# Kernel tuning notes

Hardware: AMD Instinct MI355X
Metric: run time of the kernel (lower is better)

The kernel has to match this reference:

```python
import jax, jax.numpy as jnp
import numpy as np

S = 512       # number of rnn_output rows (source positions)
T = 512       # number of target rows (queries)
DU = 512      # dim_u
DT = 512      # dim_target
D = DU + DT   # concat dim


def setup_inputs() -> dict:
    key = jax.random.key(0)
    k1, k2, k3, k4, k5, k6 = jax.random.split(key, 6)
    return {
        "rnn_outputs": jax.random.normal(k1, (S, DU), dtype=jnp.float32),
        "target": jax.random.normal(k2, (T, DT), dtype=jnp.float32),
        # nn.Linear(D, D): weight [D, D], bias [D]
        "W_lin": jax.random.normal(k3, (D, D), dtype=jnp.float32) * 0.02,
        "b_lin": jax.random.normal(k4, (D,), dtype=jnp.float32) * 0.02,
        # nn.Linear(D, 1): weight [1, D] stored flat, bias scalar
        "w_score": jax.random.normal(k5, (D,), dtype=jnp.float32) * 0.02,
        "b_score": jax.random.normal(k6, (), dtype=jnp.float32) * 0.02,
    }


def reference(rnn_outputs, target, W_lin, b_lin, w_score, b_score):
    du = rnn_outputs.shape[1]
    # linear(concat([rnn, tgt])) == rnn @ W[:, :du].T + tgt @ W[:, du:].T + b
    # (split the weight instead of materializing the [T, S, D] concat)
    A = rnn_outputs @ W_lin[:, :du].T            # [S, D]
    B = target @ W_lin[:, du:].T + b_lin         # [T, D]
    h = jnp.tanh(B[:, None, :] + A[None, :, :])  # [T, S, D]
    scores = h @ w_score + b_score               # [T, S]
    weights = jax.nn.softmax(scores, axis=1)     # softmax over source dim S
    # stack of per-row weighted sums == weights @ rnn_outputs
    return weights @ rnn_outputs                 # [T, dim_u]
```

## Files before the change

kernel.cpp:

```cpp
#include <hip/hip_runtime.h>


#define C2F 2.8853900817779268f

typedef __attribute__((ext_vector_type(8))) short short8;
typedef __attribute__((ext_vector_type(4))) float f32x4;

__device__ __forceinline__ unsigned short bf16_rne(float f) {
    unsigned u = __builtin_bit_cast(unsigned, f);
    unsigned r = (u + 0x7FFFu + ((u >> 16) & 1u)) >> 16;
    return (unsigned short)r;
}
__device__ __forceinline__ float bf16_f(unsigned short h) {
    unsigned u = ((unsigned)h) << 16;
    return __builtin_bit_cast(float, u);
}

__global__ __launch_bounds__(256, 4) void k1_mfma(
    const float* __restrict__ rnn, const float* __restrict__ tgt,
    const float* __restrict__ W, const float* __restrict__ bl,
    float* __restrict__ Abuf, float* __restrict__ Bbuf, int ksplit)
{
    __shared__ unsigned short Xh[64][40], Xl[64][40], Wh[64][40], Wl[64][40];
    const int j0 = blockIdx.x * 64;
    const int i0 = blockIdx.y * 64;
    const int kz = blockIdx.z;
    const int klen = 512 / ksplit;
    const int kbase = kz * klen;
    const bool isB = (i0 >= 512);
    const float* __restrict__ X = isB ? tgt : rnn;
    const int irow0 = isB ? (i0 - 512) : i0;
    const int koff = isB ? 512 : 0;
    const int tid = threadIdx.x;
    const int lane = tid & 63;
    const int wv = tid >> 6;
    const int isub = (wv & 1) * 32;
    const int jsub = (wv >> 1) * 32;
    const int srow = tid >> 2;
    const int skq  = tid & 3;
    const float* __restrict__ xp = X + (size_t)(irow0 + srow) * 512 + kbase + skq * 8;
    const float* __restrict__ wp = W + (size_t)(j0 + srow) * 1024 + koff + kbase + skq * 8;
    const int frow = lane & 15;
    const int fk   = (lane >> 4) * 8;
    f32x4 acc00 = {0.f,0.f,0.f,0.f}, acc01 = {0.f,0.f,0.f,0.f};
    f32x4 acc10 = {0.f,0.f,0.f,0.f}, acc11 = {0.f,0.f,0.f,0.f};
    float4 xv0 = *(const float4*)(xp);
    float4 xv1 = *(const float4*)(xp + 4);
    float4 wv0 = *(const float4*)(wp);
    float4 wv1 = *(const float4*)(wp + 4);
    for (int k0 = 0; k0 < klen; k0 += 32) {
        __syncthreads();
        {
            short8 xh8, xl8, wh8, wl8;
            const float xf[8] = {xv0.x, xv0.y, xv0.z, xv0.w, xv1.x, xv1.y, xv1.z, xv1.w};
            const float wf[8] = {wv0.x, wv0.y, wv0.z, wv0.w, wv1.x, wv1.y, wv1.z, wv1.w};
            #pragma unroll
            for (int e = 0; e < 8; ++e) {
                const unsigned short xh = bf16_rne(xf[e]);
                const unsigned short wh = bf16_rne(wf[e]);
                xh8[e] = (short)xh;
                wh8[e] = (short)wh;
                xl8[e] = (short)bf16_rne(xf[e] - bf16_f(xh));
                wl8[e] = (short)bf16_rne(wf[e] - bf16_f(wh));
            }
            *(short8*)&Xh[srow][skq * 8] = xh8;
            *(short8*)&Xl[srow][skq * 8] = xl8;
            *(short8*)&Wh[srow][skq * 8] = wh8;
            *(short8*)&Wl[srow][skq * 8] = wl8;
        }
        __syncthreads();
        if (k0 + 32 < klen) {
            xv0 = *(const float4*)(xp + k0 + 32);
            xv1 = *(const float4*)(xp + k0 + 36);
            wv0 = *(const float4*)(wp + k0 + 32);
            wv1 = *(const float4*)(wp + k0 + 36);
        }
        const short8 ah0 = *(const short8*)&Xh[isub + frow][fk];
        const short8 ah1 = *(const short8*)&Xh[isub + 16 + frow][fk];
        const short8 bh0 = *(const short8*)&Wh[jsub + frow][fk];
        const short8 bh1 = *(const short8*)&Wh[jsub + 16 + frow][fk];
        acc00 = __builtin_amdgcn_mfma_f32_16x16x32_bf16(ah0, bh0, acc00, 0, 0, 0);
        acc01 = __builtin_amdgcn_mfma_f32_16x16x32_bf16(ah0, bh1, acc01, 0, 0, 0);
        acc10 = __builtin_amdgcn_mfma_f32_16x16x32_bf16(ah1, bh0, acc10, 0, 0, 0);
        acc11 = __builtin_amdgcn_mfma_f32_16x16x32_bf16(ah1, bh1, acc11, 0, 0, 0);
        const short8 al0 = *(const short8*)&Xl[isub + frow][fk];
        const short8 al1 = *(const short8*)&Xl[isub + 16 + frow][fk];
        acc00 = __builtin_amdgcn_mfma_f32_16x16x32_bf16(al0, bh0, acc00, 0, 0, 0);
        acc01 = __builtin_amdgcn_mfma_f32_16x16x32_bf16(al0, bh1, acc01, 0, 0, 0);
        acc10 = __builtin_amdgcn_mfma_f32_16x16x32_bf16(al1, bh0, acc10, 0, 0, 0);
        acc11 = __builtin_amdgcn_mfma_f32_16x16x32_bf16(al1, bh1, acc11, 0, 0, 0);
        const short8 bl0 = *(const short8*)&Wl[jsub + frow][fk];
        const short8 bl1 = *(const short8*)&Wl[jsub + 16 + frow][fk];
        acc00 = __builtin_amdgcn_mfma_f32_16x16x32_bf16(ah0, bl0, acc00, 0, 0, 0);
        acc01 = __builtin_amdgcn_mfma_f32_16x16x32_bf16(ah0, bl1, acc01, 0, 0, 0);
        acc10 = __builtin_amdgcn_mfma_f32_16x16x32_bf16(ah1, bl0, acc10, 0, 0, 0);
        acc11 = __builtin_amdgcn_mfma_f32_16x16x32_bf16(ah1, bl1, acc11, 0, 0, 0);
    }
    const int orow = (lane >> 4) * 4;
    const int ocol = lane & 15;
    float* __restrict__ dst = (isB ? Bbuf : Abuf) + (size_t)kz * 524288;
    const bool addb = isB && (kz == ksplit - 1);
#define K1ST(ACC, MT, NT) do {                                            \
    const int jl = jsub + (NT)*16 + ocol;                                 \
    const float bb = addb ? bl[j0 + jl] : 0.f;                            \
    const int il = isub + (MT)*16 + orow;                                 \
    float* p = dst + (size_t)(irow0 + il) * 1024 + j0 + jl;               \
    p[0]    = (ACC[0] + bb) * C2F;                                        \
    p[1024] = (ACC[1] + bb) * C2F;                                        \
    p[2048] = (ACC[2] + bb) * C2F;                                        \
    p[3072] = (ACC[3] + bb) * C2F;                                        \
} while (0)
    K1ST(acc00, 0, 0); K1ST(acc01, 0, 1); K1ST(acc10, 1, 0); K1ST(acc11, 1, 1);
#undef K1ST
}

__global__ __launch_bounds__(256, 4) void k1_gemm_ab(
    const float* __restrict__ rnn, const float* __restrict__ tgt,
    const float* __restrict__ W, const float* __restrict__ bl,
    float* __restrict__ Abuf, float* __restrict__ Bbuf, int ksplit, int doexp)
{
    __shared__ float xt[32][68];
    __shared__ float wt[32][68];
    const int j0 = blockIdx.x * 64;
    const int i0 = blockIdx.y * 64;
    const int kz = blockIdx.z;
    const int klen = 512 / ksplit;
    const int kbase = kz * klen;
    const bool isB = (i0 >= 512);
    const float* __restrict__ in = isB ? tgt : rnn;
    const int irow0 = isB ? (i0 - 512) : i0;
    const int koff = isB ? 512 : 0;
    const int tid = threadIdx.x;
    const int lrow = tid >> 2;
    const int kq   = tid & 3;
    const int ti   = tid >> 4;
    const int tj   = tid & 15;
    const float* __restrict__ inp = in + (size_t)(irow0 + lrow) * 512 + kbase + kq * 8;
    const float* __restrict__ wp  = W  + (size_t)(j0 + lrow) * 1024 + koff + kbase + kq * 8;
    float acc[4][4] = {};
    float4 x0 = *(const float4*)(inp);
    float4 x1 = *(const float4*)(inp + 4);
    float4 w0 = *(const float4*)(wp);
    float4 w1 = *(const float4*)(wp + 4);
    for (int k0 = 0; k0 < klen; k0 += 32) {
        __syncthreads();
        xt[kq*8+0][lrow] = x0.x; xt[kq*8+1][lrow] = x0.y; xt[kq*8+2][lrow] = x0.z; xt[kq*8+3][lrow] = x0.w;
        xt[kq*8+4][lrow] = x1.x; xt[kq*8+5][lrow] = x1.y; xt[kq*8+6][lrow] = x1.z; xt[kq*8+7][lrow] = x1.w;
        wt[kq*8+0][lrow] = w0.x; wt[kq*8+1][lrow] = w0.y; wt[kq*8+2][lrow] = w0.z; wt[kq*8+3][lrow] = w0.w;
        wt[kq*8+4][lrow] = w1.x; wt[kq*8+5][lrow] = w1.y; wt[kq*8+6][lrow] = w1.z; wt[kq*8+7][lrow] = w1.w;
        __syncthreads();
        if (k0 + 32 < klen) {
            x0 = *(const float4*)(inp + k0 + 32);
            x1 = *(const float4*)(inp + k0 + 36);
            w0 = *(const float4*)(wp + k0 + 32);
            w1 = *(const float4*)(wp + k0 + 36);
        }
        #pragma unroll
        for (int k = 0; k < 32; ++k) {
            const float4 av = *(const float4*)&xt[k][ti * 4];
            const float4 bv = *(const float4*)&wt[k][tj * 4];
            const float ar[4] = {av.x, av.y, av.z, av.w};
            const float br[4] = {bv.x, bv.y, bv.z, bv.w};
            #pragma unroll
            for (int r = 0; r < 4; ++r)
                #pragma unroll
                for (int c = 0; c < 4; ++c)
                    acc[r][c] = __builtin_fmaf(ar[r], br[c], acc[r][c]);
        }
    }
    float4 bq = make_float4(0.f, 0.f, 0.f, 0.f);
    if (isB && kz == ksplit - 1) bq = *(const float4*)(bl + j0 + tj * 4);
    float* __restrict__ dst = (isB ? Bbuf : Abuf) + (size_t)kz * 524288;
    #pragma unroll
    for (int r = 0; r < 4; ++r) {
        float4 o;
        o.x = (acc[r][0] + bq.x) * C2F;
        o.y = (acc[r][1] + bq.y) * C2F;
        o.z = (acc[r][2] + bq.z) * C2F;
        o.w = (acc[r][3] + bq.w) * C2F;
        if (doexp) {
            o.x = __builtin_amdgcn_exp2f(o.x);
            o.y = __builtin_amdgcn_exp2f(o.y);
            o.z = __builtin_amdgcn_exp2f(o.z);
            o.w = __builtin_amdgcn_exp2f(o.w);
        }
        *(float4*)(dst + (size_t)(irow0 + ti * 4 + r) * 1024 + j0 + tj * 4) = o;
    }
}

__global__ __launch_bounds__(256, 4) void k1b_sum(float* __restrict__ ws4)
{
    const int i = (blockIdx.x * 256 + threadIdx.x) * 4;
    const float4 a0 = *(const float4*)(ws4 + i);
    const float4 a1 = *(const float4*)(ws4 + 524288 + i);
    const float4 b0 = *(const float4*)(ws4 + 2 * 524288 + i);
    const float4 b1 = *(const float4*)(ws4 + 3 * 524288 + i);
    float4 a, b;
    a.x = __builtin_amdgcn_exp2f(a0.x + a1.x);
    a.y = __builtin_amdgcn_exp2f(a0.y + a1.y);
    a.z = __builtin_amdgcn_exp2f(a0.z + a1.z);
    a.w = __builtin_amdgcn_exp2f(a0.w + a1.w);
    b.x = __builtin_amdgcn_exp2f(b0.x + b1.x);
    b.y = __builtin_amdgcn_exp2f(b0.y + b1.y);
    b.z = __builtin_amdgcn_exp2f(b0.z + b1.z);
    b.w = __builtin_amdgcn_exp2f(b0.w + b1.w);
    *(float4*)(ws4 + i) = a;
    *(float4*)(ws4 + 2 * 524288 + i) = b;
}

#define K2CELL(ACC, CC, RR) do {                                         \
    const float e0_ = __builtin_fmaf(A0.CC, B0.RR, 1.f);                 \
    const float e1_ = __builtin_fmaf(A1.CC, B1.RR, 1.f);                 \
    const float e2_ = __builtin_fmaf(A2.CC, B2.RR, 1.f);                 \
    const float e3_ = __builtin_fmaf(A3.CC, B3.RR, 1.f);                 \
    const float l01_ = e0_ * e1_;                                        \
    const float l23_ = e2_ * e3_;                                        \
    const float n01_ = __builtin_fmaf(wa.x, e1_, wa.y * e0_);            \
    const float n23_ = __builtin_fmaf(wa.z, e3_, wa.w * e2_);            \
    const float N_ = __builtin_fmaf(n01_, l23_, n23_ * l01_);            \
    ACC = __builtin_fmaf(N_, __builtin_amdgcn_rcpf(l01_ * l23_), ACC);   \
} while (0)

__global__ __launch_bounds__(256, 4) void k2_scores(
    const float* __restrict__ EA, const float* __restrict__ EB,
    const float* __restrict__ wsc, float* __restrict__ P, int dchunk)
{
    __shared__ float at[32][68];
    __shared__ float bt[32][68];
    __shared__ float wl[128];
    const int s0 = blockIdx.x * 64;
    const int t0 = blockIdx.y * 64;
    const int dz = blockIdx.z * dchunk;
    const int tid = threadIdx.x;
    if (tid < dchunk) wl[tid] = wsc[dz + tid];
    const int srow = tid & 63;
    const int kq   = tid >> 6;
    const int ti   = tid >> 4;
    const int tj   = tid & 15;
    const float* __restrict__ Arow = EA + (size_t)(s0 + srow) * 1024 + dz + kq * 8;
    const float* __restrict__ Brow = EB + (size_t)(t0 + srow) * 1024 + dz + kq * 8;
    float4 acc0 = make_float4(0.f,0.f,0.f,0.f);
    float4 acc1 = make_float4(0.f,0.f,0.f,0.f);
    float4 acc2 = make_float4(0.f,0.f,0.f,0.f);
    float4 acc3 = make_float4(0.f,0.f,0.f,0.f);
    float4 pa0 = *(const float4*)(Arow);
    float4 pa1 = *(const float4*)(Arow + 4);
    float4 pb0 = *(const float4*)(Brow);
    float4 pb1 = *(const float4*)(Brow + 4);
    for (int d0 = 0; d0 < dchunk; d0 += 32) {
        __syncthreads();
        at[kq*8+0][srow] = pa0.x; at[kq*8+1][srow] = pa0.y; at[kq*8+2][srow] = pa0.z; at[kq*8+3][srow] = pa0.w;
        at[kq*8+4][srow] = pa1.x; at[kq*8+5][srow] = pa1.y; at[kq*8+6][srow] = pa1.z; at[kq*8+7][srow] = pa1.w;
        bt[kq*8+0][srow] = pb0.x; bt[kq*8+1][srow] = pb0.y; bt[kq*8+2][srow] = pb0.z; bt[kq*8+3][srow] = pb0.w;
        bt[kq*8+4][srow] = pb1.x; bt[kq*8+5][srow] = pb1.y; bt[kq*8+6][srow] = pb1.z; bt[kq*8+7][srow] = pb1.w;
        __syncthreads();
        if (d0 + 32 < dchunk) {
            pa0 = *(const float4*)(Arow + d0 + 32);
            pa1 = *(const float4*)(Arow + d0 + 36);
            pb0 = *(const float4*)(Brow + d0 + 32);
            pb1 = *(const float4*)(Brow + d0 + 36);
        }
        for (int dd = 0; dd < 32; dd += 4) {
            const float4 wa = *(const float4*)&wl[d0 + dd];
            const float4 A0 = *(const float4*)&at[dd + 0][tj * 4];
            const float4 A1 = *(const float4*)&at[dd + 1][tj * 4];
            const float4 A2 = *(const float4*)&at[dd + 2][tj * 4];
            const float4 A3 = *(const float4*)&at[dd + 3][tj * 4];
            const float4 B0 = *(const float4*)&bt[dd + 0][ti * 4];
            const float4 B1 = *(const float4*)&bt[dd + 1][ti * 4];
            const float4 B2 = *(const float4*)&bt[dd + 2][ti * 4];
            const float4 B3 = *(const float4*)&bt[dd + 3][ti * 4];
            K2CELL(acc0.x, x, x); K2CELL(acc0.y, y, x); K2CELL(acc0.z, z, x); K2CELL(acc0.w, w, x);
            K2CELL(acc1.x, x, y); K2CELL(acc1.y, y, y); K2CELL(acc1.z, z, y); K2CELL(acc1.w, w, y);
            K2CELL(acc2.x, x, z); K2CELL(acc2.y, y, z); K2CELL(acc2.z, z, z); K2CELL(acc2.w, w, z);
            K2CELL(acc3.x, x, w); K2CELL(acc3.y, y, w); K2CELL(acc3.z, z, w); K2CELL(acc3.w, w, w);
        }
    }
    float* __restrict__ Pz = P + (size_t)blockIdx.z * 512 * 512;
    *(float4*)(Pz + (size_t)(t0 + ti * 4 + 0) * 512 + s0 + tj * 4) = acc0;
    *(float4*)(Pz + (size_t)(t0 + ti * 4 + 1) * 512 + s0 + tj * 4) = acc1;
    *(float4*)(Pz + (size_t)(t0 + ti * 4 + 2) * 512 + s0 + tj * 4) = acc2;
    *(float4*)(Pz + (size_t)(t0 + ti * 4 + 3) * 512 + s0 + tj * 4) = acc3;
}

__global__ __launch_bounds__(256, 4) void k3_softmax(
    const float* __restrict__ P, float* __restrict__ wgt, int nz)
{
    __shared__ float wm[4];
    __shared__ float wsum[4];
    const int t = blockIdx.x;
    const int tid = threadIdx.x;
    const size_t base = (size_t)t * 512 + tid * 2;
    float sx = 0.f, sy = 0.f;
    for (int z = 0; z < nz; ++z) {
        const float2 p = *(const float2*)(P + base + (size_t)z * 262144);
        sx += p.x; sy += p.y;
    }
    const float x0 = -2.f * sx;
    const float x1 = -2.f * sy;
    float m = fmaxf(x0, x1);
    #pragma unroll
    for (int off = 32; off; off >>= 1) m = fmaxf(m, __shfl_xor(m, off));
    if ((tid & 63) == 0) wm[tid >> 6] = m;
    __syncthreads();
    m = fmaxf(fmaxf(wm[0], wm[1]), fmaxf(wm[2], wm[3]));
    const float L2E = 1.4426950408889634f;
    const float e0 = __builtin_amdgcn_exp2f((x0 - m) * L2E);
    const float e1 = __builtin_amdgcn_exp2f((x1 - m) * L2E);
    float s = e0 + e1;
    #pragma unroll
    for (int off = 32; off; off >>= 1) s += __shfl_xor(s, off);
    if ((tid & 63) == 0) wsum[tid >> 6] = s;
    __syncthreads();
    s = wsum[0] + wsum[1] + wsum[2] + wsum[3];
    const float inv = 1.0f / s;
    float2 o; o.x = e0 * inv; o.y = e1 * inv;
    *(float2*)(wgt + (size_t)t * 512 + tid * 2) = o;
}

__global__ __launch_bounds__(256, 4) void k4_out(
    const float* __restrict__ wgt, const float* __restrict__ rnn,
    float* __restrict__ P4)
{
    __shared__ float wtt[32][68];
    __shared__ float rn[32][68];
    const int d0g = blockIdx.x * 64;
    const int t0g = blockIdx.y * 64;
    const int z   = blockIdx.z;
    const int tid = threadIdx.x;
    const int trow = tid & 63;
    const int kq   = tid >> 6;
    const int srw  = tid & 31;
    const int cq   = tid >> 5;
    const int ti = tid >> 4, tj = tid & 15;
    float acc[4][4] = {};
    for (int sc = z * 64; sc < z * 64 + 64; sc += 32) {
        const float4 w0 = *(const float4*)(wgt + (size_t)(t0g + trow) * 512 + sc + kq * 8);
        const float4 w1 = *(const float4*)(wgt + (size_t)(t0g + trow) * 512 + sc + kq * 8 + 4);
        const float4 r0 = *(const float4*)(rnn + (size_t)(sc + srw) * 512 + d0g + cq * 8);
        const float4 r1 = *(const float4*)(rnn + (size_t)(sc + srw) * 512 + d0g + cq * 8 + 4);
        __syncthreads();
        wtt[kq*8+0][trow] = w0.x; wtt[kq*8+1][trow] = w0.y; wtt[kq*8+2][trow] = w0.z; wtt[kq*8+3][trow] = w0.w;
        wtt[kq*8+4][trow] = w1.x; wtt[kq*8+5][trow] = w1.y; wtt[kq*8+6][trow] = w1.z; wtt[kq*8+7][trow] = w1.w;
        *(float4*)&rn[srw][cq * 8]     = r0;
        *(float4*)&rn[srw][cq * 8 + 4] = r1;
        __syncthreads();
        #pragma unroll
        for (int s = 0; s < 32; ++s) {
            const float4 av = *(const float4*)&wtt[s][ti * 4];
            const float4 bv = *(const float4*)&rn[s][tj * 4];
            const float ar[4] = {av.x, av.y, av.z, av.w};
            const float bc[4] = {bv.x, bv.y, bv.z, bv.w};
            #pragma unroll
            for (int r = 0; r < 4; ++r)
                #pragma unroll
                for (int c = 0; c < 4; ++c)
                    acc[r][c] = __builtin_fmaf(ar[r], bc[c], acc[r][c]);
        }
    }
    float* __restrict__ Pz = P4 + (size_t)z * 262144;
    #pragma unroll
    for (int r = 0; r < 4; ++r) {
        float4 o;
        o.x = acc[r][0]; o.y = acc[r][1]; o.z = acc[r][2]; o.w = acc[r][3];
        *(float4*)(Pz + (size_t)(t0g + ti * 4 + r) * 512 + d0g + tj * 4) = o;
    }
}

__global__ __launch_bounds__(256, 4) void k5_reduce(
    const float* __restrict__ P4, float* __restrict__ out)
{
    const int i = (blockIdx.x * 256 + threadIdx.x) * 4;
    float4 a = *(const float4*)(P4 + i);
    #pragma unroll
    for (int z = 1; z < 8; ++z) {
        const float4 b = *(const float4*)(P4 + (size_t)z * 262144 + i);
        a.x += b.x; a.y += b.y; a.z += b.z; a.w += b.w;
    }
    *(float4*)(out + i) = a;
}

extern "C" void kernel_launch(void* const* d_in, const int* in_sizes, int n_in,
                              void* d_out, int out_size, void* d_ws, size_t ws_size,
                              hipStream_t stream) {
    const float* rnn = (const float*)d_in[0];
    const float* tgt = (const float*)d_in[1];
    const float* W   = (const float*)d_in[2];
    const float* bl  = (const float*)d_in[3];
    const float* wsc = (const float*)d_in[4];
    float* out = (float*)d_out;

    const int nz = 8;
    const int dchunk = 1024 / nz;
    float* ws = (float*)d_ws;

    const bool split = (ws_size >= 17825792u);

    if (split) {
        float* A   = ws;
        float* B   = ws + 2 * 524288;
        float* P   = ws + 4 * 524288;
        float* wgt = P + (size_t)nz * 262144;
        float* P4  = P;
        k1_mfma   <<<dim3(16, 16, 2), 256, 0, stream>>>(rnn, tgt, W, bl, A, B, 2);
        k1b_sum   <<<512,             256, 0, stream>>>(ws);
        k2_scores <<<dim3(8, 8, nz),  256, 0, stream>>>(A, B, wsc, P, dchunk);
        k3_softmax<<<512,             256, 0, stream>>>(P, wgt, nz);
        k4_out    <<<dim3(8, 8, 8),   256, 0, stream>>>(wgt, rnn, P4);
        k5_reduce <<<256,             256, 0, stream>>>(P4, out);
    } else {
        float* A   = ws;
        float* B   = ws + 524288;
        float* P   = ws + 2 * 524288;
        float* wgt = P + (size_t)nz * 262144;
        float* P4  = P;
        k1_gemm_ab<<<dim3(16, 16, 1), 256, 0, stream>>>(rnn, tgt, W, bl, A, B, 1, 1);
        k2_scores <<<dim3(8, 8, nz),  256, 0, stream>>>(A, B, wsc, P, dchunk);
        k3_softmax<<<512,             256, 0, stream>>>(P, wgt, nz);
        k4_out    <<<dim3(8, 8, 8),   256, 0, stream>>>(wgt, rnn, P4);
        k5_reduce <<<256,             256, 0, stream>>>(P4, out);
    }
}
```

Before: 59.96 us.

## Fuse split-K sum and exp into score kernel; use bf16x3 MFMA for output GEMM

Removes the separate k1b_sum kernel. The score kernel now loads both split-K partials of A and B, adds them, and applies exp2 while staging into shared memory. This saves one launch and a full read-write pass over the workspace, but the exp is now recomputed in every score block that reads the same data. The weights@rnn kernel is also rewritten to use bf16 MFMA with hi/lo splitting (three products) in place of scalar FMA, trading conversion overhead for matrix-core throughput.

```diff
diff --git a/kernel.cpp b/kernel.cpp
--- a/kernel.cpp
+++ b/kernel.cpp
@@ -188,26 +188,6 @@
     }
 }
 
-__global__ __launch_bounds__(256, 4) void k1b_sum(float* __restrict__ ws4)
-{
-    const int i = (blockIdx.x * 256 + threadIdx.x) * 4;
-    const float4 a0 = *(const float4*)(ws4 + i);
-    const float4 a1 = *(const float4*)(ws4 + 524288 + i);
-    const float4 b0 = *(const float4*)(ws4 + 2 * 524288 + i);
-    const float4 b1 = *(const float4*)(ws4 + 3 * 524288 + i);
-    float4 a, b;
-    a.x = __builtin_amdgcn_exp2f(a0.x + a1.x);
-    a.y = __builtin_amdgcn_exp2f(a0.y + a1.y);
-    a.z = __builtin_amdgcn_exp2f(a0.z + a1.z);
-    a.w = __builtin_amdgcn_exp2f(a0.w + a1.w);
-    b.x = __builtin_amdgcn_exp2f(b0.x + b1.x);
-    b.y = __builtin_amdgcn_exp2f(b0.y + b1.y);
-    b.z = __builtin_amdgcn_exp2f(b0.z + b1.z);
-    b.w = __builtin_amdgcn_exp2f(b0.w + b1.w);
-    *(float4*)(ws4 + i) = a;
-    *(float4*)(ws4 + 2 * 524288 + i) = b;
-}
-
 #define K2CELL(ACC, CC, RR) do {                                         \
     const float e0_ = __builtin_fmaf(A0.CC, B0.RR, 1.f);                 \
     const float e1_ = __builtin_fmaf(A1.CC, B1.RR, 1.f);                 \
@@ -221,9 +201,12 @@
     ACC = __builtin_fmaf(N_, __builtin_amdgcn_rcpf(l01_ * l23_), ACC);   \
 } while (0)
 
+#define K2EXP(P0, P1) __builtin_amdgcn_exp2f(__builtin_fmaf(sumf, (P1), (P0)))
+
 __global__ __launch_bounds__(256, 4) void k2_scores(
-    const float* __restrict__ EA, const float* __restrict__ EB,
-    const float* __restrict__ wsc, float* __restrict__ P, int dchunk)
+    const float* __restrict__ A0p, const float* __restrict__ A1p,
+    const float* __restrict__ B0p, const float* __restrict__ B1p,
+    const float* __restrict__ wsc, float* __restrict__ P, int dchunk, float sumf)
 {
     __shared__ float at[32][68];
     __shared__ float bt[32][68];
@@ -237,28 +220,50 @@
     const int kq   = tid >> 6;
     const int ti   = tid >> 4;
     const int tj   = tid & 15;
-    const float* __restrict__ Arow = EA + (size_t)(s0 + srow) * 1024 + dz + kq * 8;
-    const float* __restrict__ Brow = EB + (size_t)(t0 + srow) * 1024 + dz + kq * 8;
+    const float* __restrict__ Ar0 = A0p + (size_t)(s0 + srow) * 1024 + dz + kq * 8;
+    const float* __restrict__ Ar1 = A1p + (size_t)(s0 + srow) * 1024 + dz + kq * 8;
+    const float* __restrict__ Br0 = B0p + (size_t)(t0 + srow) * 1024 + dz + kq * 8;
+    const float* __restrict__ Br1 = B1p + (size_t)(t0 + srow) * 1024 + dz + kq * 8;
     float4 acc0 = make_float4(0.f,0.f,0.f,0.f);
     float4 acc1 = make_float4(0.f,0.f,0.f,0.f);
     float4 acc2 = make_float4(0.f,0.f,0.f,0.f);
     float4 acc3 = make_float4(0.f,0.f,0.f,0.f);
-    float4 pa0 = *(const float4*)(Arow);
-    float4 pa1 = *(const float4*)(Arow + 4);
-    float4 pb0 = *(const float4*)(Brow);
-    float4 pb1 = *(const float4*)(Brow + 4);
+    float4 pa0 = *(const float4*)(Ar0);
+    float4 pa0b = *(const float4*)(Ar0 + 4);
+    float4 pa1 = *(const float4*)(Ar1);
+    float4 pa1b = *(const float4*)(Ar1 + 4);
+    float4 pb0 = *(const float4*)(Br0);
+    float4 pb0b = *(const float4*)(Br0 + 4);
+    float4 pb1 = *(const float4*)(Br1);
+    float4 pb1b = *(const float4*)(Br1 + 4);
     for (int d0 = 0; d0 < dchunk; d0 += 32) {
         __syncthreads();
-        at[kq*8+0][srow] = pa0.x; at[kq*8+1][srow] = pa0.y; at[kq*8+2][srow] = pa0.z; at[kq*8+3][srow] = pa0.w;
-        at[kq*8+4][srow] = pa1.x; at[kq*8+5][srow] = pa1.y; at[kq*8+6][srow] = pa1.z; at[kq*8+7][srow] = pa1.w;
-        bt[kq*8+0][srow] = pb0.x; bt[kq*8+1][srow] = pb0.y; bt[kq*8+2][srow] = pb0.z; bt[kq*8+3][srow] = pb0.w;
-        bt[kq*8+4][srow] = pb1.x; bt[kq*8+5][srow] = pb1.y; bt[kq*8+6][srow] = pb1.z; bt[kq*8+7][srow] = pb1.w;
+        at[kq*8+0][srow] = K2EXP(pa0.x,  pa1.x);
+        at[kq*8+1][srow] = K2EXP(pa0.y,  pa1.y);
+        at[kq*8+2][srow] = K2EXP(pa0.z,  pa1.z);
+        at[kq*8+3][srow] = K2EXP(pa0.w,  pa1.w);
+        at[kq*8+4][srow] = K2EXP(pa0b.x, pa1b.x);
+        at[kq*8+5][srow] = K2EXP(pa0b.y, pa1b.y);
+        at[kq*8+6][srow] = K2EXP(pa0b.z, pa1b.z);
+        at[kq*8+7][srow] = K2EXP(pa0b.w, pa1b.w);
+        bt[kq*8+0][srow] = K2EXP(pb0.x,  pb1.x);
+        bt[kq*8+1][srow] = K2EXP(pb0.y,  pb1.y);
+        bt[kq*8+2][srow] = K2EXP(pb0.z,  pb1.z);
+        bt[kq*8+3][srow] = K2EXP(pb0.w,  pb1.w);
+        bt[kq*8+4][srow] = K2EXP(pb0b.x, pb1b.x);
+        bt[kq*8+5][srow] = K2EXP(pb0b.y, pb1b.y);
+        bt[kq*8+6][srow] = K2EXP(pb0b.z, pb1b.z);
+        bt[kq*8+7][srow] = K2EXP(pb0b.w, pb1b.w);
         __syncthreads();
         if (d0 + 32 < dchunk) {
-            pa0 = *(const float4*)(Arow + d0 + 32);
-            pa1 = *(const float4*)(Arow + d0 + 36);
-            pb0 = *(const float4*)(Brow + d0 + 32);
-            pb1 = *(const float4*)(Brow + d0 + 36);
+            pa0  = *(const float4*)(Ar0 + d0 + 32);
+            pa0b = *(const float4*)(Ar0 + d0 + 36);
+            pa1  = *(const float4*)(Ar1 + d0 + 32);
+            pa1b = *(const float4*)(Ar1 + d0 + 36);
+            pb0  = *(const float4*)(Br0 + d0 + 32);
+            pb0b = *(const float4*)(Br0 + d0 + 36);
+            pb1  = *(const float4*)(Br1 + d0 + 32);
+            pb1b = *(const float4*)(Br1 + d0 + 36);
         }
         for (int dd = 0; dd < 32; dd += 4) {
             const float4 wa = *(const float4*)&wl[d0 + dd];
@@ -318,53 +323,101 @@
     *(float2*)(wgt + (size_t)t * 512 + tid * 2) = o;
 }
 
-__global__ __launch_bounds__(256, 4) void k4_out(
+#define K4BFRAG(BH, BL, DCOL) do {                                      \
+    _Pragma("unroll")                                                   \
+    for (int e = 0; e < 8; ++e) {                                       \
+        const float v_ = rs[fk + e][(DCOL)];                            \
+        const unsigned short h_ = bf16_rne(v_);                         \
+        (BH)[e] = (short)h_;                                            \
+        (BL)[e] = (short)bf16_rne(v_ - bf16_f(h_));                     \
+    }                                                                   \
+} while (0)
+
+__global__ __launch_bounds__(256, 4) void k4_mfma(
     const float* __restrict__ wgt, const float* __restrict__ rnn,
     float* __restrict__ P4)
 {
-    __shared__ float wtt[32][68];
-    __shared__ float rn[32][68];
+    __shared__ unsigned short Gh[64][40], Gl[64][40];
+    __shared__ float rs[32][69];
     const int d0g = blockIdx.x * 64;
     const int t0g = blockIdx.y * 64;
     const int z   = blockIdx.z;
     const int tid = threadIdx.x;
-    const int trow = tid & 63;
-    const int kq   = tid >> 6;
-    const int srw  = tid & 31;
-    const int cq   = tid >> 5;
-    const int ti = tid >> 4, tj = tid & 15;
-    float acc[4][4] = {};
-    for (int sc = z * 64; sc < z * 64 + 64; sc += 32) {
-        const float4 w0 = *(const float4*)(wgt + (size_t)(t0g + trow) * 512 + sc + kq * 8);
-        const float4 w1 = *(const float4*)(wgt + (size_t)(t0g + trow) * 512 + sc + kq * 8 + 4);
-        const float4 r0 = *(const float4*)(rnn + (size_t)(sc + srw) * 512 + d0g + cq * 8);
-        const float4 r1 = *(const float4*)(rnn + (size_t)(sc + srw) * 512 + d0g + cq * 8 + 4);
-        __syncthreads();
-        wtt[kq*8+0][trow] = w0.x; wtt[kq*8+1][trow] = w0.y; wtt[kq*8+2][trow] = w0.z; wtt[kq*8+3][trow] = w0.w;
-        wtt[kq*8+4][trow] = w1.x; wtt[kq*8+5][trow] = w1.y; wtt[kq*8+6][trow] = w1.z; wtt[kq*8+7][trow] = w1.w;
-        *(float4*)&rn[srw][cq * 8]     = r0;
-        *(float4*)&rn[srw][cq * 8 + 4] = r1;
-        __syncthreads();
-        #pragma unroll
-        for (int s = 0; s < 32; ++s) {
-            const float4 av = *(const float4*)&wtt[s][ti * 4];
-            const float4 bv = *(const float4*)&rn[s][tj * 4];
-            const float ar[4] = {av.x, av.y, av.z, av.w};
-            const float bc[4] = {bv.x, bv.y, bv.z, bv.w};
+    const int lane = tid & 63;
+    const int wv = tid >> 6;
+    const int tsub = (wv & 1) * 32;
+    const int dsub = (wv >> 1) * 32;
+    const int trow = tid >> 2, skq = tid & 3;
+    const int srw  = tid >> 3, cq  = tid & 7;
+    const int frow = lane & 15;
+    const int fk   = (lane >> 4) * 8;
+    const int sbase = z * 64;
+    f32x4 acc00 = {0.f,0.f,0.f,0.f}, acc01 = {0.f,0.f,0.f,0.f};
+    f32x4 acc10 = {0.f,0.f,0.f,0.f}, acc11 = {0.f,0.f,0.f,0.f};
+    const float* __restrict__ gp = wgt + (size_t)(t0g + trow) * 512 + sbase + skq * 8;
+    const float* __restrict__ rp = rnn + (size_t)(sbase + srw) * 512 + d0g + cq * 8;
+    float4 g0 = *(const float4*)(gp);
+    float4 g1 = *(const float4*)(gp + 4);
+    float4 r0 = *(const float4*)(rp);
+    float4 r1 = *(const float4*)(rp + 4);
+    #pragma unroll
+    for (int c = 0; c < 2; ++c) {
+        __syncthreads();
+        {
+            short8 gh8, gl8;
+            const float gf[8] = {g0.x,g0.y,g0.z,g0.w,g1.x,g1.y,g1.z,g1.w};
             #pragma unroll
-            for (int r = 0; r < 4; ++r)
-                #pragma unroll
-                for (int c = 0; c < 4; ++c)
-                    acc[r][c] = __builtin_fmaf(ar[r], bc[c], acc[r][c]);
-        }
-    }
+            for (int e = 0; e < 8; ++e) {
+                const unsigned short h = bf16_rne(gf[e]);
+                gh8[e] = (short)h;
+                gl8[e] = (short)bf16_rne(gf[e] - bf16_f(h));
+            }
+            *(short8*)&Gh[trow][skq * 8] = gh8;
+            *(short8*)&Gl[trow][skq * 8] = gl8;
+            *(float4*)&rs[srw][cq * 8]     = r0;
+            *(float4*)&rs[srw][cq * 8 + 4] = r1;
+        }
+        __syncthreads();
+        if (c == 0) {
+            g0 = *(const float4*)(gp + 32);
+            g1 = *(const float4*)(gp + 36);
+            r0 = *(const float4*)(rp + 32 * 512);
+            r1 = *(const float4*)(rp + 32 * 512 + 4);
+        }
+        const short8 ah0 = *(const short8*)&Gh[tsub + frow][fk];
+        const short8 ah1 = *(const short8*)&Gh[tsub + 16 + frow][fk];
+        const short8 al0 = *(const short8*)&Gl[tsub + frow][fk];
+        const short8 al1 = *(const short8*)&Gl[tsub + 16 + frow][fk];
+        short8 bh0, bl0, bh1, bl1;
+        K4BFRAG(bh0, bl0, dsub + frow);
+        K4BFRAG(bh1, bl1, dsub + 16 + frow);
+        acc00 = __builtin_amdgcn_mfma_f32_16x16x32_bf16(ah0, bh0, acc00, 0, 0, 0);
+        acc01 = __builtin_amdgcn_mfma_f32_16x16x32_bf16(ah0, bh1, acc01, 0, 0, 0);
+        acc10 = __builtin_amdgcn_mfma_f32_16x16x32_bf16(ah1, bh0, acc10, 0, 0, 0);
+        acc11 = __builtin_amdgcn_mfma_f32_16x16x32_bf16(ah1, bh1, acc11, 0, 0, 0);
+        acc00 = __builtin_amdgcn_mfma_f32_16x16x32_bf16(al0, bh0, acc00, 0, 0, 0);
+        acc01 = __builtin_amdgcn_mfma_f32_16x16x32_bf16(al0, bh1, acc01, 0, 0, 0);
+        acc10 = __builtin_amdgcn_mfma_f32_16x16x32_bf16(al1, bh0, acc10, 0, 0, 0);
+        acc11 = __builtin_amdgcn_mfma_f32_16x16x32_bf16(al1, bh1, acc11, 0, 0, 0);
+        acc00 = __builtin_amdgcn_mfma_f32_16x16x32_bf16(ah0, bl0, acc00, 0, 0, 0);
+        acc01 = __builtin_amdgcn_mfma_f32_16x16x32_bf16(ah0, bl1, acc01, 0, 0, 0);
+        acc10 = __builtin_amdgcn_mfma_f32_16x16x32_bf16(ah1, bl0, acc10, 0, 0, 0);
+        acc11 = __builtin_amdgcn_mfma_f32_16x16x32_bf16(ah1, bl1, acc11, 0, 0, 0);
+    }
+    const int orow = (lane >> 4) * 4;
+    const int ocol = lane & 15;
     float* __restrict__ Pz = P4 + (size_t)z * 262144;
-    #pragma unroll
-    for (int r = 0; r < 4; ++r) {
-        float4 o;
-        o.x = acc[r][0]; o.y = acc[r][1]; o.z = acc[r][2]; o.w = acc[r][3];
-        *(float4*)(Pz + (size_t)(t0g + ti * 4 + r) * 512 + d0g + tj * 4) = o;
-    }
+#define K4ST(ACC, MT, NT) do {                                           \
+    const int tl = tsub + (MT)*16 + orow;                                \
+    const int dl = dsub + (NT)*16 + ocol;                                \
+    float* p = Pz + (size_t)(t0g + tl) * 512 + d0g + dl;                 \
+    p[0]    = ACC[0];                                                    \
+    p[512]  = ACC[1];                                                    \
+    p[1024] = ACC[2];                                                    \
+    p[1536] = ACC[3];                                                    \
+} while (0)
+    K4ST(acc00, 0, 0); K4ST(acc01, 0, 1); K4ST(acc10, 1, 0); K4ST(acc11, 1, 1);
+#undef K4ST
 }
 
 __global__ __launch_bounds__(256, 4) void k5_reduce(
@@ -403,10 +456,10 @@
         float* wgt = P + (size_t)nz * 262144;
         float* P4  = P;
         k1_mfma   <<<dim3(16, 16, 2), 256, 0, stream>>>(rnn, tgt, W, bl, A, B, 2);
-        k1b_sum   <<<512,             256, 0, stream>>>(ws);
-        k2_scores <<<dim3(8, 8, nz),  256, 0, stream>>>(A, B, wsc, P, dchunk);
+        k2_scores <<<dim3(8, 8, nz),  256, 0, stream>>>(A, A + 524288, B, B + 524288,
+                                                        wsc, P, dchunk, 1.f);
         k3_softmax<<<512,             256, 0, stream>>>(P, wgt, nz);
-        k4_out    <<<dim3(8, 8, 8),   256, 0, stream>>>(wgt, rnn, P4);
+        k4_mfma   <<<dim3(8, 8, 8),   256, 0, stream>>>(wgt, rnn, P4);
         k5_reduce <<<256,             256, 0, stream>>>(P4, out);
     } else {
         float* A   = ws;
@@ -414,10 +467,10 @@
         float* P   = ws + 2 * 524288;
         float* wgt = P + (size_t)nz * 262144;
         float* P4  = P;
-        k1_gemm_ab<<<dim3(16, 16, 1), 256, 0, stream>>>(rnn, tgt, W, bl, A, B, 1, 1);
-        k2_scores <<<dim3(8, 8, nz),  256, 0, stream>>>(A, B, wsc, P, dchunk);
+        k1_gemm_ab<<<dim3(16, 16, 1), 256, 0, stream>>>(rnn, tgt, W, bl, A, B, 1, 0);
+        k2_scores <<<dim3(8, 8, nz),  256, 0, stream>>>(A, A, B, B, wsc, P, dchunk, 0.f);
         k3_softmax<<<512,             256, 0, stream>>>(P, wgt, nz);
-        k4_out    <<<dim3(8, 8, 8),   256, 0, stream>>>(wgt, rnn, P4);
+        k4_mfma   <<<dim3(8, 8, 8),   256, 0, stream>>>(wgt, rnn, P4);
         k5_reduce <<<256,             256, 0, stream>>>(P4, out);
     }
 }
```

After: 57.49 us. -4.1%, faster.
